# Optimization experiments

Measured on AMD Instinct MI355X. Metric: run time of the kernel, lower is better.

## Reference

```python
import jax, jax.numpy as jnp
import numpy as np

N = 10000   # nodes
E = 80000   # edges per graph (avg degree 8)
H = 32      # hidden width (hard-coded in module)
VD0 = 2048  # visual_dim for gcn_0
VD1 = 256   # visual_dim // 8 for gcn_b21


def setup_inputs() -> dict:
    key = jax.random.key(0)
    ks = jax.random.split(key, 16)
    rn = lambda k, s, sc=1.0: jax.random.normal(k, s, dtype=jnp.float32) * sc
    return {
        "x": rn(ks[0], (N, 9)),
        "vis0": rn(ks[1], (N, VD0)),
        "vis1": rn(ks[2], (N, VD1)),
        "edge_index0": jax.random.randint(ks[3], (2, E), 0, N),
        "edge_index1": jax.random.randint(ks[4], (2, E), 0, N),
        # input_mlp: Linear(9,32) -> BatchNorm1d(32) (eval) -> PReLU -> Dropout(0) -> Linear(32,32)
        "W_in1": rn(ks[5], (9, H), 0.3), "b_in1": jnp.zeros((H,), jnp.float32),
        "bn_gamma": jnp.ones((H,), jnp.float32), "bn_beta": jnp.zeros((H,), jnp.float32),
        "bn_mean": jnp.zeros((H,), jnp.float32), "bn_var": jnp.ones((H,), jnp.float32),
        "prelu_a": jnp.asarray(0.25, jnp.float32),
        "W_in2": rn(ks[6], (H, H), 0.15), "b_in2": jnp.zeros((H,), jnp.float32),
        "w_node": rn(ks[7], (H, 1), 0.15), "b_node": jnp.zeros((1,), jnp.float32),
        "W_c0": rn(ks[8], (H, H), 0.15), "b_c0": jnp.zeros((H,), jnp.float32),
        "W_c1": rn(ks[9], (H, H), 0.15), "b_c1": jnp.zeros((H,), jnp.float32),
        "w_p0": rn(ks[10], (H, 1), 0.15), "b_p0": jnp.zeros((1,), jnp.float32),
        "w_p1": rn(ks[11], (H, 1), 0.15), "b_p1": jnp.zeros((1,), jnp.float32),
    }


def _cm_cos_conv(h, edge_index, vis, W, b):
    # gather-weight-scatter: w_e = cos(vis[src], vis[dst]); out_i = (sum_e->i w_e * h[src_e]) @ W + b
    src, dst = edge_index[0], edge_index[1]
    vn = vis * jax.lax.rsqrt(jnp.sum(vis * vis, axis=-1, keepdims=True) + 1e-8)
    w = jnp.sum(vn[src] * vn[dst], axis=-1)  # [E] cosine similarity per edge
    agg = jax.ops.segment_sum(h[src] * w[:, None], dst, num_segments=h.shape[0])  # [N,H]
    return agg @ W + b  # conv_activation=None -> identity


def reference(x, vis0, vis1, edge_index0, edge_index1, W_in1, b_in1, bn_gamma, bn_beta, bn_mean, bn_var, prelu_a, W_in2, b_in2, w_node, b_node, W_c0, b_c0, W_c1, b_c1, w_p0, b_p0, w_p1, b_p1):
    h = x @ W_in1 + b_in1
    h = bn_gamma * (h - bn_mean) * jax.lax.rsqrt(bn_var + 1e-5) + bn_beta
    h = jnp.where(h >= 0, h, prelu_a * h)  # PReLU (single shared slope)
    h = h @ W_in2 + b_in2                   # [N,32] shared for graphs 0 and 4
    nodes_scores = (h @ w_node + b_node)[:, 0]
    h0 = _cm_cos_conv(h, edge_index0, vis0, W_c0, b_c0)
    h1 = _cm_cos_conv(h, edge_index1, vis1, W_c1, b_c1)
    s0 = (h0 @ w_p0 + b_p0)[:, 0]
    s1 = (h1 @ w_p1 + b_p1)[:, 0]
    return nodes_scores + s0 + s1
```

## Files before the change

kernel.cpp:

```cpp
#include <hip/hip_runtime.h>

#define N_NODES 10000
#define NE      80000
#define H       32
#define VD0     2048
#define VD1     256

#define NODE_BLOCKS  40
#define NC_BLOCKS    2500
#define HIST_BLOCKS  313
#define PREP_BLOCKS  (NODE_BLOCKS + 2 * NC_BLOCKS + HIST_BLOCKS)

#define EDGE0_BLOCKS 10000
#define EDGE1_BLOCKS 2500
#define EDGE_BLOCKS  (EDGE0_BLOCKS + EDGE1_BLOCKS)

__device__ inline unsigned short f2bf_rne(float f) {
    unsigned int u = __float_as_uint(f);
    u += 0x7fffu + ((u >> 16) & 1u);
    return (unsigned short)(u >> 16);
}
__device__ inline float bflo(unsigned int u) { return __uint_as_float(u << 16); }
__device__ inline float bfhi(unsigned int u) { return __uint_as_float(u & 0xffff0000u); }

__device__ inline float dot8_bf16(uint4 a, uint4 b) {
    float s;
    s  = bflo(a.x) * bflo(b.x) + bfhi(a.x) * bfhi(b.x);
    s += bflo(a.y) * bflo(b.y) + bfhi(a.y) * bfhi(b.y);
    s += bflo(a.z) * bflo(b.z) + bfhi(a.z) * bfhi(b.z);
    s += bflo(a.w) * bflo(b.w) + bfhi(a.w) * bfhi(b.w);
    return s;
}
__device__ inline float dot4_bf16(uint2 a, uint2 b) {
    return bflo(a.x) * bflo(b.x) + bfhi(a.x) * bfhi(b.x)
         + bflo(a.y) * bflo(b.y) + bfhi(a.y) * bfhi(b.y);
}

template <int VD>
__device__ inline void normconv_node(const float* __restrict__ vis,
                                     unsigned short* __restrict__ vn,
                                     int node, int lane)
{
    const float4* v = (const float4*)(vis + (size_t)node * VD);
    float4 f[VD / 256];
    float acc = 0.f;
    #pragma unroll
    for (int it = 0; it < VD / 256; it++) {
        f[it] = v[it * 64 + lane];
        acc += f[it].x * f[it].x + f[it].y * f[it].y + f[it].z * f[it].z + f[it].w * f[it].w;
    }
    #pragma unroll
    for (int o = 32; o; o >>= 1) acc += __shfl_xor(acc, o);
    const float inv = rsqrtf(acc + 1e-8f);
    ushort4* o4 = (ushort4*)(vn + (size_t)node * VD);
    #pragma unroll
    for (int it = 0; it < VD / 256; it++) {
        ushort4 r;
        r.x = f2bf_rne(f[it].x * inv);
        r.y = f2bf_rne(f[it].y * inv);
        r.z = f2bf_rne(f[it].z * inv);
        r.w = f2bf_rne(f[it].w * inv);
        o4[it * 64 + lane] = r;
    }
}

__global__ __launch_bounds__(256) void prep_kernel(
    const float* __restrict__ x,
    const float* __restrict__ vis0, const float* __restrict__ vis1,
    const int* __restrict__ ei0, const int* __restrict__ ei1,
    const float* __restrict__ W_in1, const float* __restrict__ b_in1,
    const float* __restrict__ bn_gamma, const float* __restrict__ bn_beta,
    const float* __restrict__ bn_mean, const float* __restrict__ bn_var,
    const float* __restrict__ prelu_a,
    const float* __restrict__ W_in2, const float* __restrict__ b_in2,
    const float* __restrict__ w_node, const float* __restrict__ b_node,
    const float* __restrict__ W_c0, const float* __restrict__ b_c0,
    const float* __restrict__ W_c1, const float* __restrict__ b_c1,
    const float* __restrict__ w_p0, const float* __restrict__ b_p0,
    const float* __restrict__ w_p1, const float* __restrict__ b_p1,
    float* __restrict__ out, float* __restrict__ p0w, float* __restrict__ p1w,
    unsigned short* __restrict__ vn0, unsigned short* __restrict__ vn1,
    int* __restrict__ deg0, int* __restrict__ deg1)
{
    const int bid = blockIdx.x;
    const int t   = threadIdx.x;

    if (bid < NODE_BLOCKS) {
        __shared__ float sW1[9 * H];
        __shared__ float sW2[H * H];
        __shared__ float sU0[H], sU1[H], sWn[H];
        __shared__ float sB1[H], sB2[H], sSc[H], sSh[H];
        __shared__ float sC;

        for (int i = t; i < 9 * H; i += 256) sW1[i] = W_in1[i];
        for (int i = t; i < H * H; i += 256) sW2[i] = W_in2[i];
        if (t < H) {
            sB1[t] = b_in1[t];
            sB2[t] = b_in2[t];
            float sc = bn_gamma[t] * rsqrtf(bn_var[t] + 1e-5f);
            sSc[t] = sc;
            sSh[t] = bn_beta[t] - bn_mean[t] * sc;
            sWn[t] = w_node[t];
            float u0 = 0.f, u1 = 0.f;
            for (int j = 0; j < H; j++) {
                u0 += W_c0[t * H + j] * w_p0[j];
                u1 += W_c1[t * H + j] * w_p1[j];
            }
            sU0[t] = u0; sU1[t] = u1;
        }
        if (t == 0) {
            float c0 = b_p0[0], c1 = b_p1[0];
            for (int j = 0; j < H; j++) { c0 += b_c0[j] * w_p0[j]; c1 += b_c1[j] * w_p1[j]; }
            sC = c0 + c1 + b_node[0];
        }
        __syncthreads();

        const float a = prelu_a[0];
        const int n = bid * 256 + t;
        if (n >= N_NODES) return;

        float xi[9];
        #pragma unroll
        for (int i = 0; i < 9; i++) xi[i] = x[n * 9 + i];

        float tt[H];
        #pragma unroll
        for (int j = 0; j < H; j++) {
            float s = sB1[j];
            #pragma unroll
            for (int i = 0; i < 9; i++) s += xi[i] * sW1[i * H + j];
            s = s * sSc[j] + sSh[j];
            tt[j] = s >= 0.f ? s : a * s;
        }

        float ns = 0.f, p0 = 0.f, p1 = 0.f;
        #pragma unroll
        for (int k = 0; k < H; k++) {
            float h = sB2[k];
            #pragma unroll
            for (int j = 0; j < H; j++) h += tt[j] * sW2[j * H + k];
            ns += h * sWn[k];
            p0 += h * sU0[k];
            p1 += h * sU1[k];
        }
        out[n] = ns + sC;
        p0w[n] = p0;
        p1w[n] = p1;
    } else if (bid < NODE_BLOCKS + NC_BLOCKS) {
        const int node = ((bid - NODE_BLOCKS) * 256 + t) >> 6;
        if (node < N_NODES) normconv_node<VD0>(vis0, vn0, node, t & 63);
    } else if (bid < NODE_BLOCKS + 2 * NC_BLOCKS) {
        const int node = ((bid - NODE_BLOCKS - NC_BLOCKS) * 256 + t) >> 6;
        if (node < N_NODES) normconv_node<VD1>(vis1, vn1, node, t & 63);
    } else {
        const int e = (bid - NODE_BLOCKS - 2 * NC_BLOCKS) * 256 + t;
        if (e < NE) {
            atomicAdd(&deg0[ei0[NE + e]], 1);
            atomicAdd(&deg1[ei1[NE + e]], 1);
        }
    }
}

__global__ __launch_bounds__(1024) void scan_kernel(
    const int* __restrict__ deg0, int* __restrict__ row0, int* __restrict__ cur0,
    const int* __restrict__ deg1, int* __restrict__ row1, int* __restrict__ cur1)
{
    const int* deg = blockIdx.x ? deg1 : deg0;
    int* row_start = blockIdx.x ? row1 : row0;
    int* cursor    = blockIdx.x ? cur1 : cur0;

    __shared__ int s[1024];
    const int t = threadIdx.x;
    const int base = t * 10;
    int local[10];
    int sum = 0;
    #pragma unroll
    for (int k = 0; k < 10; k++) {
        int v = (base + k < N_NODES) ? deg[base + k] : 0;
        local[k] = v;
        sum += v;
    }
    s[t] = sum;
    __syncthreads();
    for (int off = 1; off < 1024; off <<= 1) {
        int v = 0;
        if (t >= off) v = s[t - off];
        __syncthreads();
        if (t >= off) s[t] += v;
        __syncthreads();
    }
    int excl = s[t] - sum;
    #pragma unroll
    for (int k = 0; k < 10; k++) {
        if (base + k < N_NODES) {
            row_start[base + k] = excl;
            cursor[base + k] = excl;
            excl += local[k];
        }
    }
    if (t == 1023) row_start[N_NODES] = s[1023];
}

__global__ __launch_bounds__(256) void scatter_kernel(
    const int* __restrict__ ei0, int* __restrict__ cur0, int* __restrict__ csr0,
    const int* __restrict__ ei1, int* __restrict__ cur1, int* __restrict__ csr1)
{
    const int e = blockIdx.x * 256 + threadIdx.x;
    if (e < NE) {
        int d = ei0[NE + e];
        csr0[atomicAdd(&cur0[d], 1)] = ei0[e];
        d = ei1[NE + e];
        csr1[atomicAdd(&cur1[d], 1)] = ei1[e];
    }
}

__global__ __launch_bounds__(256) void edge_kernel_fused(
    const unsigned short* __restrict__ vn0,
    const int* __restrict__ row0, const int* __restrict__ csr0,
    const float* __restrict__ p0w,
    const unsigned short* __restrict__ vn1,
    const int* __restrict__ row1, const int* __restrict__ csr1,
    const float* __restrict__ p1w,
    float* __restrict__ out)
{
    const int bid  = blockIdx.x;
    const int lane = threadIdx.x & 63;

    if (bid < EDGE0_BLOCKS) {
        const int d = bid;
        const int w = threadIdx.x >> 6;
        const int beg = row0[d];
        const int end = row0[d + 1];
        __shared__ float sred[4];

        float partial = 0.f;
        if (beg != end) {
            const uint4* pd = (const uint4*)(vn0 + (size_t)d * VD0 + w * 512);
            const uint4 dreg = pd[lane];
            int j = beg;
            for (; j + 3 < end; j += 4) {
                const int s0 = csr0[j], s1 = csr0[j + 1], s2 = csr0[j + 2], s3 = csr0[j + 3];
                const uint4 r0 = ((const uint4*)(vn0 + (size_t)s0 * VD0 + w * 512))[lane];
                const uint4 r1 = ((const uint4*)(vn0 + (size_t)s1 * VD0 + w * 512))[lane];
                const uint4 r2 = ((const uint4*)(vn0 + (size_t)s2 * VD0 + w * 512))[lane];
                const uint4 r3 = ((const uint4*)(vn0 + (size_t)s3 * VD0 + w * 512))[lane];
                partial += dot8_bf16(dreg, r0) * p0w[s0];
                partial += dot8_bf16(dreg, r1) * p0w[s1];
                partial += dot8_bf16(dreg, r2) * p0w[s2];
                partial += dot8_bf16(dreg, r3) * p0w[s3];
            }
            for (; j < end; j++) {
                const int s0 = csr0[j];
                const uint4 r0 = ((const uint4*)(vn0 + (size_t)s0 * VD0 + w * 512))[lane];
                partial += dot8_bf16(dreg, r0) * p0w[s0];
            }
        }
        #pragma unroll
        for (int o = 32; o; o >>= 1) partial += __shfl_down(partial, o);
        if (lane == 0) sred[w] = partial;
        __syncthreads();
        if (threadIdx.x == 0 && beg != end) {
            atomicAdd(&out[d], sred[0] + sred[1] + sred[2] + sred[3]);
        }
    } else {
        const int d = (bid - EDGE0_BLOCKS) * 4 + (threadIdx.x >> 6);
        const int beg = row1[d];
        const int end = row1[d + 1];
        if (beg == end) return;
        const uint2 dreg = ((const uint2*)(vn1 + (size_t)d * VD1))[lane];
        float partial = 0.f;
        int j = beg;
        for (; j + 3 < end; j += 4) {
            const int s0 = csr1[j], s1 = csr1[j + 1], s2 = csr1[j + 2], s3 = csr1[j + 3];
            const uint2 r0 = ((const uint2*)(vn1 + (size_t)s0 * VD1))[lane];
            const uint2 r1 = ((const uint2*)(vn1 + (size_t)s1 * VD1))[lane];
            const uint2 r2 = ((const uint2*)(vn1 + (size_t)s2 * VD1))[lane];
            const uint2 r3 = ((const uint2*)(vn1 + (size_t)s3 * VD1))[lane];
            partial += dot4_bf16(dreg, r0) * p1w[s0];
            partial += dot4_bf16(dreg, r1) * p1w[s1];
            partial += dot4_bf16(dreg, r2) * p1w[s2];
            partial += dot4_bf16(dreg, r3) * p1w[s3];
        }
        for (; j < end; j++) {
            const int s0 = csr1[j];
            const uint2 r0 = ((const uint2*)(vn1 + (size_t)s0 * VD1))[lane];
            partial += dot4_bf16(dreg, r0) * p1w[s0];
        }
        #pragma unroll
        for (int o = 32; o; o >>= 1) partial += __shfl_down(partial, o);
        if (lane == 0) atomicAdd(&out[d], partial);
    }
}

template <int VD>
__global__ __launch_bounds__(256) void norm_kernel(const float* __restrict__ vis,
                                                   float* __restrict__ inv)
{
    const int wave = (blockIdx.x * 256 + threadIdx.x) >> 6;
    const int lane = threadIdx.x & 63;
    if (wave >= N_NODES) return;
    const float4* v = (const float4*)(vis + (size_t)wave * VD);
    float acc = 0.f;
    #pragma unroll
    for (int it = 0; it < VD / 256; it++) {
        float4 f = v[lane + it * 64];
        acc += f.x * f.x + f.y * f.y + f.z * f.z + f.w * f.w;
    }
    #pragma unroll
    for (int o = 32; o; o >>= 1) acc += __shfl_down(acc, o);
    if (lane == 0) inv[wave] = rsqrtf(acc + 1e-8f);
}

template <int VD>
__global__ __launch_bounds__(256) void edge_kernel(
    const float* __restrict__ vis, const int* __restrict__ ei,
    const float* __restrict__ inv, const float* __restrict__ p,
    float* __restrict__ out)
{
    const int wave = (blockIdx.x * 256 + threadIdx.x) >> 6;
    const int lane = threadIdx.x & 63;
    if (wave >= NE) return;
    const int src = ei[wave];
    const int dst = ei[NE + wave];
    const float4* va = (const float4*)(vis + (size_t)src * VD);
    const float4* vb = (const float4*)(vis + (size_t)dst * VD);
    float acc = 0.f;
    #pragma unroll
    for (int it = 0; it < VD / 256; it++) {
        float4 fa = va[lane + it * 64];
        float4 fb = vb[lane + it * 64];
        acc += fa.x * fb.x + fa.y * fb.y + fa.z * fb.z + fa.w * fb.w;
    }
    #pragma unroll
    for (int o = 32; o; o >>= 1) acc += __shfl_down(acc, o);
    if (lane == 0) {
        float w = acc * inv[src] * inv[dst];
        atomicAdd(&out[dst], w * p[src]);
    }
}

__global__ __launch_bounds__(256) void node_kernel_fb(
    const float* __restrict__ x,
    const float* __restrict__ W_in1, const float* __restrict__ b_in1,
    const float* __restrict__ bn_gamma, const float* __restrict__ bn_beta,
    const float* __restrict__ bn_mean, const float* __restrict__ bn_var,
    const float* __restrict__ prelu_a,
    const float* __restrict__ W_in2, const float* __restrict__ b_in2,
    const float* __restrict__ w_node, const float* __restrict__ b_node,
    const float* __restrict__ W_c0, const float* __restrict__ b_c0,
    const float* __restrict__ W_c1, const float* __restrict__ b_c1,
    const float* __restrict__ w_p0, const float* __restrict__ b_p0,
    const float* __restrict__ w_p1, const float* __restrict__ b_p1,
    float* __restrict__ out, float* __restrict__ p0w, float* __restrict__ p1w)
{
    __shared__ float sW1[9 * H];
    __shared__ float sW2[H * H];
    __shared__ float sU0[H], sU1[H], sWn[H];
    __shared__ float sB1[H], sB2[H], sSc[H], sSh[H];
    __shared__ float sC;

    const int t = threadIdx.x;
    for (int i = t; i < 9 * H; i += 256) sW1[i] = W_in1[i];
    for (int i = t; i < H * H; i += 256) sW2[i] = W_in2[i];
    if (t < H) {
        sB1[t] = b_in1[t];
        sB2[t] = b_in2[t];
        float sc = bn_gamma[t] * rsqrtf(bn_var[t] + 1e-5f);
        sSc[t] = sc;
        sSh[t] = bn_beta[t] - bn_mean[t] * sc;
        sWn[t] = w_node[t];
        float u0 = 0.f, u1 = 0.f;
        for (int j = 0; j < H; j++) {
            u0 += W_c0[t * H + j] * w_p0[j];
            u1 += W_c1[t * H + j] * w_p1[j];
        }
        sU0[t] = u0; sU1[t] = u1;
    }
    if (t == 0) {
        float c0 = b_p0[0], c1 = b_p1[0];
        for (int j = 0; j < H; j++) { c0 += b_c0[j] * w_p0[j]; c1 += b_c1[j] * w_p1[j]; }
        sC = c0 + c1 + b_node[0];
    }
    __syncthreads();

    const float a = prelu_a[0];
    const int n = blockIdx.x * 256 + t;
    if (n >= N_NODES) return;

    float xi[9];
    #pragma unroll
    for (int i = 0; i < 9; i++) xi[i] = x[n * 9 + i];

    float tt[H];
    #pragma unroll
    for (int j = 0; j < H; j++) {
        float s = sB1[j];
        #pragma unroll
        for (int i = 0; i < 9; i++) s += xi[i] * sW1[i * H + j];
        s = s * sSc[j] + sSh[j];
        tt[j] = s >= 0.f ? s : a * s;
    }

    float ns = 0.f, p0 = 0.f, p1 = 0.f;
    #pragma unroll
    for (int k = 0; k < H; k++) {
        float h = sB2[k];
        #pragma unroll
        for (int j = 0; j < H; j++) h += tt[j] * sW2[j * H + k];
        ns += h * sWn[k];
        p0 += h * sU0[k];
        p1 += h * sU1[k];
    }
    out[n] = ns + sC;
    p0w[n] = p0;
    p1w[n] = p1;
}

extern "C" void kernel_launch(void* const* d_in, const int* in_sizes, int n_in,
                              void* d_out, int out_size, void* d_ws, size_t ws_size,
                              hipStream_t stream)
{
    const float* x        = (const float*)d_in[0];
    const float* vis0     = (const float*)d_in[1];
    const float* vis1     = (const float*)d_in[2];
    const int*   ei0      = (const int*)d_in[3];
    const int*   ei1      = (const int*)d_in[4];
    const float* W_in1    = (const float*)d_in[5];
    const float* b_in1    = (const float*)d_in[6];
    const float* bn_gamma = (const float*)d_in[7];
    const float* bn_beta  = (const float*)d_in[8];
    const float* bn_mean  = (const float*)d_in[9];
    const float* bn_var   = (const float*)d_in[10];
    const float* prelu_a  = (const float*)d_in[11];
    const float* W_in2    = (const float*)d_in[12];
    const float* b_in2    = (const float*)d_in[13];
    const float* w_node   = (const float*)d_in[14];
    const float* b_node   = (const float*)d_in[15];
    const float* W_c0     = (const float*)d_in[16];
    const float* b_c0     = (const float*)d_in[17];
    const float* W_c1     = (const float*)d_in[18];
    const float* b_c1     = (const float*)d_in[19];
    const float* w_p0     = (const float*)d_in[20];
    const float* b_p0     = (const float*)d_in[21];
    const float* w_p1     = (const float*)d_in[22];
    const float* b_p1     = (const float*)d_in[23];

    float* out = (float*)d_out;

    char* ws = (char*)d_ws;
    float* p0w  = (float*)ws;                  ws += N_NODES * 4;
    float* p1w  = (float*)ws;                  ws += N_NODES * 4;
    float* inv0 = (float*)ws;                  ws += N_NODES * 4;
    float* inv1 = (float*)ws;                  ws += N_NODES * 4;
    int* deg0       = (int*)ws;                ws += N_NODES * 4;
    int* deg1       = (int*)ws;                ws += N_NODES * 4;
    int* row0       = (int*)ws;                ws += (N_NODES + 1) * 4;
    int* row1       = (int*)ws;                ws += (N_NODES + 1) * 4;
    int* cur0       = (int*)ws;                ws += N_NODES * 4;
    int* cur1       = (int*)ws;                ws += N_NODES * 4;
    int* csr0       = (int*)ws;                ws += NE * 4;
    int* csr1       = (int*)ws;                ws += NE * 4;
    unsigned short* vn0 = (unsigned short*)ws; ws += (size_t)N_NODES * VD0 * 2;
    unsigned short* vn1 = (unsigned short*)ws; ws += (size_t)N_NODES * VD1 * 2;
    const size_t need = (size_t)(ws - (char*)d_ws);

    if (ws_size >= need) {
        hipMemsetAsync(deg0, 0, 2 * N_NODES * sizeof(int), stream);

        prep_kernel<<<PREP_BLOCKS, 256, 0, stream>>>(
            x, vis0, vis1, ei0, ei1,
            W_in1, b_in1, bn_gamma, bn_beta, bn_mean, bn_var, prelu_a,
            W_in2, b_in2, w_node, b_node, W_c0, b_c0, W_c1, b_c1,
            w_p0, b_p0, w_p1, b_p1,
            out, p0w, p1w, vn0, vn1, deg0, deg1);

        scan_kernel<<<2, 1024, 0, stream>>>(deg0, row0, cur0, deg1, row1, cur1);

        scatter_kernel<<<(NE + 255) / 256, 256, 0, stream>>>(
            ei0, cur0, csr0, ei1, cur1, csr1);

        edge_kernel_fused<<<EDGE_BLOCKS, 256, 0, stream>>>(
            vn0, row0, csr0, p0w, vn1, row1, csr1, p1w, out);
    } else {
        node_kernel_fb<<<(N_NODES + 255) / 256, 256, 0, stream>>>(
            x, W_in1, b_in1, bn_gamma, bn_beta, bn_mean, bn_var, prelu_a,
            W_in2, b_in2, w_node, b_node, W_c0, b_c0, W_c1, b_c1,
            w_p0, b_p0, w_p1, b_p1, out, p0w, p1w);
        norm_kernel<VD0><<<(N_NODES * 64 + 255) / 256, 256, 0, stream>>>(vis0, inv0);
        norm_kernel<VD1><<<(N_NODES * 64 + 255) / 256, 256, 0, stream>>>(vis1, inv1);
        edge_kernel<VD0><<<(NE * 64 + 255) / 256, 256, 0, stream>>>(vis0, ei0, inv0, p0w, out);
        edge_kernel<VD1><<<(NE * 64 + 255) / 256, 256, 0, stream>>>(vis1, ei1, inv1, p1w, out);
    }
}
```

Baseline: 261.6 us.

## Split graph-0 edge work into feature-chunk phases with one destination per wave

Previously each block handled one destination node, with its four waves covering the four 512-element chunks of the 2048-wide visual vector and combining through shared memory and a barrier. Now blocks are grouped into four phases by feature chunk, and each wave handles a different destination within one chunk, issuing its own atomicAdd. The aim is for concurrently running blocks to touch the same 1 KB slice of source rows so that L2 reuse improves, and to remove the shared-memory reduction and barrier. The cost is four times as many atomic adds per node, plus extra load imbalance between waves when degrees differ.

```diff
diff --git a/kernel.cpp b/kernel.cpp
--- a/kernel.cpp
+++ b/kernel.cpp
@@ -11,9 +11,11 @@
 #define HIST_BLOCKS  313
 #define PREP_BLOCKS  (NODE_BLOCKS + 2 * NC_BLOCKS + HIST_BLOCKS)
 
-#define EDGE0_BLOCKS 10000
-#define EDGE1_BLOCKS 2500
-#define EDGE_BLOCKS  (EDGE0_BLOCKS + EDGE1_BLOCKS)
+#define EDGE0_PHASES  4
+#define EDGE0_GBLK    2500
+#define EDGE0_BLOCKS  (EDGE0_PHASES * EDGE0_GBLK)
+#define EDGE1_BLOCKS  2500
+#define EDGE_BLOCKS   (EDGE0_BLOCKS + EDGE1_BLOCKS)
 
 __device__ inline unsigned short f2bf_rne(float f) {
     unsigned int u = __float_as_uint(f);
@@ -227,41 +229,36 @@
     const int lane = threadIdx.x & 63;
 
     if (bid < EDGE0_BLOCKS) {
-        const int d = bid;
-        const int w = threadIdx.x >> 6;
+        const int phase = bid / EDGE0_GBLK;
+        const int group = bid % EDGE0_GBLK;
+        const int d     = group * 4 + (threadIdx.x >> 6);
+        const int koff  = phase * 512;
         const int beg = row0[d];
         const int end = row0[d + 1];
-        __shared__ float sred[4];
-
+        if (beg == end) return;
+
+        const uint4 dreg = ((const uint4*)(vn0 + (size_t)d * VD0 + koff))[lane];
         float partial = 0.f;
-        if (beg != end) {
-            const uint4* pd = (const uint4*)(vn0 + (size_t)d * VD0 + w * 512);
-            const uint4 dreg = pd[lane];
-            int j = beg;
-            for (; j + 3 < end; j += 4) {
-                const int s0 = csr0[j], s1 = csr0[j + 1], s2 = csr0[j + 2], s3 = csr0[j + 3];
-                const uint4 r0 = ((const uint4*)(vn0 + (size_t)s0 * VD0 + w * 512))[lane];
-                const uint4 r1 = ((const uint4*)(vn0 + (size_t)s1 * VD0 + w * 512))[lane];
-                const uint4 r2 = ((const uint4*)(vn0 + (size_t)s2 * VD0 + w * 512))[lane];
-                const uint4 r3 = ((const uint4*)(vn0 + (size_t)s3 * VD0 + w * 512))[lane];
-                partial += dot8_bf16(dreg, r0) * p0w[s0];
-                partial += dot8_bf16(dreg, r1) * p0w[s1];
-                partial += dot8_bf16(dreg, r2) * p0w[s2];
-                partial += dot8_bf16(dreg, r3) * p0w[s3];
-            }
-            for (; j < end; j++) {
-                const int s0 = csr0[j];
-                const uint4 r0 = ((const uint4*)(vn0 + (size_t)s0 * VD0 + w * 512))[lane];
-                partial += dot8_bf16(dreg, r0) * p0w[s0];
-            }
+        int j = beg;
+        for (; j + 3 < end; j += 4) {
+            const int s0 = csr0[j], s1 = csr0[j + 1], s2 = csr0[j + 2], s3 = csr0[j + 3];
+            const uint4 r0 = ((const uint4*)(vn0 + (size_t)s0 * VD0 + koff))[lane];
+            const uint4 r1 = ((const uint4*)(vn0 + (size_t)s1 * VD0 + koff))[lane];
+            const uint4 r2 = ((const uint4*)(vn0 + (size_t)s2 * VD0 + koff))[lane];
+            const uint4 r3 = ((const uint4*)(vn0 + (size_t)s3 * VD0 + koff))[lane];
+            partial += dot8_bf16(dreg, r0) * p0w[s0];
+            partial += dot8_bf16(dreg, r1) * p0w[s1];
+            partial += dot8_bf16(dreg, r2) * p0w[s2];
+            partial += dot8_bf16(dreg, r3) * p0w[s3];
+        }
+        for (; j < end; j++) {
+            const int s0 = csr0[j];
+            const uint4 r0 = ((const uint4*)(vn0 + (size_t)s0 * VD0 + koff))[lane];
+            partial += dot8_bf16(dreg, r0) * p0w[s0];
         }
         #pragma unroll
         for (int o = 32; o; o >>= 1) partial += __shfl_down(partial, o);
-        if (lane == 0) sred[w] = partial;
-        __syncthreads();
-        if (threadIdx.x == 0 && beg != end) {
-            atomicAdd(&out[d], sred[0] + sred[1] + sred[2] + sred[3]);
-        }
+        if (lane == 0) atomicAdd(&out[d], partial);
     } else {
         const int d = (bid - EDGE0_BLOCKS) * 4 + (threadIdx.x >> 6);
         const int beg = row1[d];
```

Result: faster. 255.2 us (median of 2 runs) (-2.5%).
